# Kernel optimization log

Measured on AMD Instinct MI355X. Metric: run time of the kernel, lower is better.

## Reference

```python
import jax, jax.numpy as jnp
import numpy as np
import math

DIM = 4096
N_HEADS = 32
N_KV_HEADS = 8
HEAD_DIM = DIM // N_HEADS  # 128
ROPE_THETA = 500000.0
SEQ_LEN = 1
START_IDX = 8191
CACHE_LEN = START_IDX + SEQ_LEN  # 8192


def _rope(x, cos, sin):
    # x: [s, h, d]; cos/sin: [s, d//2]. Strided (even/odd) RoPE as in source.
    xe = x[:, :, 0::2]
    xo = x[:, :, 1::2]
    c = cos[:, None, :]
    s = sin[:, None, :]
    re = xe * c - xo * s
    ro = xe * s + xo * c
    # interleave back: [..., d//2, 2] -> [..., d]
    return jnp.stack([re, ro], axis=-1).reshape(x.shape)


def setup_inputs() -> dict:
    key = jax.random.key(0)
    ks = jax.random.split(key, 7)
    sc = 0.02
    return {
        "x": jax.random.normal(ks[0], (SEQ_LEN, DIM), jnp.float32),
        "wq": jax.random.normal(ks[1], (DIM, DIM), jnp.float32) * sc,
        "wk": jax.random.normal(ks[2], (N_KV_HEADS * HEAD_DIM, DIM), jnp.float32) * sc,
        "wv": jax.random.normal(ks[3], (N_KV_HEADS * HEAD_DIM, DIM), jnp.float32) * sc,
        "wo": jax.random.normal(ks[4], (DIM, DIM), jnp.float32) * sc,
        "k_cache": jax.random.normal(ks[5], (CACHE_LEN, N_KV_HEADS, HEAD_DIM), jnp.float32),
        "v_cache": jax.random.normal(ks[6], (CACHE_LEN, N_KV_HEADS, HEAD_DIM), jnp.float32),
        "start_idx": START_IDX,
    }


def reference(x, wq, wk, wv, wo, k_cache, v_cache, start_idx):
    seq_len = x.shape[0]
    # QKV projections (matmul with w.T as in source)
    Q = (x @ wq.T).reshape(seq_len, N_HEADS, HEAD_DIM)
    K = (x @ wk.T).reshape(seq_len, N_KV_HEADS, HEAD_DIM)
    V = (x @ wv.T).reshape(seq_len, N_KV_HEADS, HEAD_DIM)

    # RoPE frequencies for positions [start_idx, start_idx+seq_len)
    inv_freq = 1.0 / (ROPE_THETA ** (jnp.arange(0, HEAD_DIM, 2, dtype=jnp.float32) / HEAD_DIM))
    t = jnp.arange(start_idx, start_idx + seq_len, dtype=jnp.float32)
    freqs = t[:, None] * inv_freq[None, :]  # [s, d/2]
    cos, sin = jnp.cos(freqs), jnp.sin(freqs)

    Q = _rope(Q, cos, sin)
    K = _rope(K, cos, sin)

    # KV-cache append (start_idx is a static Python int)
    kc = jax.lax.dynamic_update_slice(k_cache, K, (start_idx, 0, 0))
    vc = jax.lax.dynamic_update_slice(v_cache, V, (start_idx, 0, 0))
    total = start_idx + seq_len
    keys = kc[:total]    # [T, kvh, d]
    values = vc[:total]

    rep = N_HEADS // N_KV_HEADS
    Kr = jnp.repeat(keys, rep, axis=1)    # [T, h, d] (repeat_interleave)
    Vr = jnp.repeat(values, rep, axis=1)

    scale = 1.0 / math.sqrt(HEAD_DIM)
    scores = jnp.einsum('qhd,khd->hqk', Q, Kr) * scale  # [h, s, T]

    if seq_len > 1:
        q_pos = jnp.arange(seq_len)[:, None] + start_idx
        k_pos = jnp.arange(total)[None, :]
        mask = jnp.where(k_pos > q_pos, jnp.float32(-jnp.inf), 0.0)
        scores = scores + mask[None, :, :]

    probs = jax.nn.softmax(scores.astype(jnp.float32), axis=-1).astype(Q.dtype)
    out = jnp.einsum('hqk,khd->qhd', probs, Vr).reshape(seq_len, N_HEADS * HEAD_DIM)
    return out @ wo.T
```

## Files before the change

kernel.cpp:

```cpp
#include <hip/hip_runtime.h>
#include <math.h>

#define DIM 4096
#define HD 128
#define NH 32
#define NKV 8
#define CACHE_LEN 8192
#define NCHUNK 64
#define CHUNK 128
#define SCALE 0.08838834764831845f

__global__ __launch_bounds__(256) void qkv_rope_kernel(
    const float* __restrict__ x, const float* __restrict__ wq,
    const float* __restrict__ wk, const float* __restrict__ wv,
    float* __restrict__ k_cache, float* __restrict__ v_cache,
    const int* __restrict__ start_idx_p, float* __restrict__ q_out)
{
    const int wave = threadIdx.x >> 6;
    const int lane = threadIdx.x & 63;
    const int row  = blockIdx.x * 4 + wave;

    const float* w;
    if (row < DIM)                w = wq + (size_t)row * DIM;
    else if (row < DIM + NKV*HD)  w = wk + (size_t)(row - DIM) * DIM;
    else                          w = wv + (size_t)(row - DIM - NKV*HD) * DIM;

    const float4* w4 = (const float4*)w;
    const float4* x4 = (const float4*)x;
    float acc = 0.f;
#pragma unroll
    for (int it = 0; it < DIM/4/64; ++it) {
        float4 a = w4[it*64 + lane];
        float4 b = x4[it*64 + lane];
        acc = fmaf(a.x, b.x, acc); acc = fmaf(a.y, b.y, acc);
        acc = fmaf(a.z, b.z, acc); acc = fmaf(a.w, b.w, acc);
    }
#pragma unroll
    for (int off = 32; off > 0; off >>= 1) acc += __shfl_down(acc, off);

    __shared__ float dots[4];
    if (lane == 0) dots[wave] = acc;
    __syncthreads();

    if (threadIdx.x < 2) {
        const int sidx = *start_idx_p;
        const int r0 = blockIdx.x * 4 + (int)threadIdx.x * 2;
        const float de = dots[threadIdx.x*2];
        const float dd = dots[threadIdx.x*2 + 1];
        if (r0 < DIM + NKV*HD) {
            const int local = (r0 < DIM) ? r0 : r0 - DIM;
            const int p = (local & (HD-1)) >> 1;
            const float te   = (float)pow(500000.0, (double)p * (1.0/64.0));
            const float invf = 1.0f / te;
            const float freq = (float)sidx * invf;
            const double ang = (double)freq;
            const float c = (float)cos(ang), s = (float)sin(ang);
            const float re = de * c - dd * s;
            const float ro = de * s + dd * c;
            if (r0 < DIM) {
                q_out[r0] = re; q_out[r0+1] = ro;
            } else {
                const size_t base = (size_t)sidx * (NKV*HD) + (size_t)(r0 - DIM);
                k_cache[base] = re; k_cache[base+1] = ro;
            }
        } else {
            const size_t base = (size_t)sidx * (NKV*HD) + (size_t)(r0 - DIM - NKV*HD);
            v_cache[base] = de; v_cache[base+1] = dd;
        }
    }
}

__global__ __launch_bounds__(256) void attn_partial_kernel(
    const float* __restrict__ q, const float* __restrict__ k_cache,
    const float* __restrict__ v_cache,
    float* __restrict__ part_acc,
    float* __restrict__ part_l)
{
    const int kv    = blockIdx.x >> 6;
    const int chunk = blockIdx.x & 63;
    const int wave  = threadIdx.x >> 6;
    const int lane  = threadIdx.x & 63;
    const int g  = lane >> 4;
    const int gl = lane & 15;

    float4 q0[4], q1[4];
#pragma unroll
    for (int hh = 0; hh < 4; ++hh) {
        const float* qb = q + (size_t)(kv*4 + hh) * HD;
        float4 a = *(const float4*)(qb + gl*4);
        float4 b = *(const float4*)(qb + 64 + gl*4);
        a.x *= SCALE; a.y *= SCALE; a.z *= SCALE; a.w *= SCALE;
        b.x *= SCALE; b.y *= SCALE; b.z *= SCALE; b.w *= SCALE;
        q0[hh] = a; q1[hh] = b;
    }

    float acc0[4][4] = {{0}}, acc1[4][4] = {{0}};
    float lsum[4] = {0.f, 0.f, 0.f, 0.f};

    const int pbase = chunk*CHUNK + wave*32 + g;
    for (int it = 0; it < 8; ++it) {
        const int pos = pbase + it*4;
        const float* kb = k_cache + ((size_t)pos*NKV + kv) * HD;
        float4 k0 = *(const float4*)(kb + gl*4);
        float4 k1 = *(const float4*)(kb + 64 + gl*4);
        float s[4];
#pragma unroll
        for (int hh = 0; hh < 4; ++hh) {
            float t;
            t = q0[hh].x*k0.x + q0[hh].y*k0.y + q0[hh].z*k0.z + q0[hh].w*k0.w;
            t += q1[hh].x*k1.x + q1[hh].y*k1.y + q1[hh].z*k1.z + q1[hh].w*k1.w;
            s[hh] = t;
        }
#pragma unroll
        for (int off = 1; off < 16; off <<= 1) {
#pragma unroll
            for (int hh = 0; hh < 4; ++hh) s[hh] += __shfl_xor(s[hh], off);
        }
        const float* vb = v_cache + ((size_t)pos*NKV + kv) * HD;
        float4 v0 = *(const float4*)(vb + gl*4);
        float4 v1 = *(const float4*)(vb + 64 + gl*4);
#pragma unroll
        for (int hh = 0; hh < 4; ++hh) {
            const float p = expf(s[hh]);
            lsum[hh] += p;
            acc0[hh][0] = fmaf(p, v0.x, acc0[hh][0]);
            acc0[hh][1] = fmaf(p, v0.y, acc0[hh][1]);
            acc0[hh][2] = fmaf(p, v0.z, acc0[hh][2]);
            acc0[hh][3] = fmaf(p, v0.w, acc0[hh][3]);
            acc1[hh][0] = fmaf(p, v1.x, acc1[hh][0]);
            acc1[hh][1] = fmaf(p, v1.y, acc1[hh][1]);
            acc1[hh][2] = fmaf(p, v1.z, acc1[hh][2]);
            acc1[hh][3] = fmaf(p, v1.w, acc1[hh][3]);
        }
    }

#pragma unroll
    for (int off = 16; off < 64; off <<= 1) {
#pragma unroll
        for (int hh = 0; hh < 4; ++hh) {
            lsum[hh] += __shfl_xor(lsum[hh], off);
#pragma unroll
            for (int j = 0; j < 4; ++j) {
                acc0[hh][j] += __shfl_xor(acc0[hh][j], off);
                acc1[hh][j] += __shfl_xor(acc1[hh][j], off);
            }
        }
    }

    __shared__ float red[4][4*HD];
    __shared__ float lred[4][4];
    if (lane < 16) {
#pragma unroll
        for (int hh = 0; hh < 4; ++hh) {
            *(float4*)&red[wave][hh*HD + gl*4] =
                make_float4(acc0[hh][0], acc0[hh][1], acc0[hh][2], acc0[hh][3]);
            *(float4*)&red[wave][hh*HD + 64 + gl*4] =
                make_float4(acc1[hh][0], acc1[hh][1], acc1[hh][2], acc1[hh][3]);
        }
        if (gl == 0) {
            lred[wave][0] = lsum[0]; lred[wave][1] = lsum[1];
            lred[wave][2] = lsum[2]; lred[wave][3] = lsum[3];
        }
    }
    __syncthreads();

    float* outp = part_acc + (size_t)blockIdx.x * (4*HD);
#pragma unroll
    for (int k = 0; k < 2; ++k) {
        const int idx = (int)threadIdx.x + k*256;
        outp[idx] = red[0][idx] + red[1][idx] + red[2][idx] + red[3][idx];
    }
    if (threadIdx.x < 4) {
        part_l[(size_t)blockIdx.x*4 + threadIdx.x] =
            lred[0][threadIdx.x] + lred[1][threadIdx.x] +
            lred[2][threadIdx.x] + lred[3][threadIdx.x];
    }
}

__global__ __launch_bounds__(128) void attn_combine_kernel(
    const float* __restrict__ part_acc, const float* __restrict__ part_l,
    float* __restrict__ attn_out)
{
    const int h  = blockIdx.x;
    const int kv = h >> 2, hh = h & 3;
    const int d  = threadIdx.x;
    float acc = 0.f, l = 0.f;
    for (int c = 0; c < NCHUNK; ++c) {
        const int pid = kv*NCHUNK + c;
        acc += part_acc[(size_t)pid*(4*HD) + hh*HD + d];
        l   += part_l[pid*4 + hh];
    }
    attn_out[h*HD + d] = acc / l;
}

__global__ __launch_bounds__(256) void out_proj_kernel(
    const float* __restrict__ attn, const float* __restrict__ wo,
    float* __restrict__ out)
{
    const int wave = threadIdx.x >> 6;
    const int lane = threadIdx.x & 63;
    const int row  = blockIdx.x * 4 + wave;
    const float4* w4 = (const float4*)(wo + (size_t)row * DIM);
    const float4* a4 = (const float4*)attn;
    float acc = 0.f;
#pragma unroll
    for (int it = 0; it < DIM/4/64; ++it) {
        float4 a = w4[it*64 + lane];
        float4 b = a4[it*64 + lane];
        acc = fmaf(a.x, b.x, acc); acc = fmaf(a.y, b.y, acc);
        acc = fmaf(a.z, b.z, acc); acc = fmaf(a.w, b.w, acc);
    }
#pragma unroll
    for (int off = 32; off > 0; off >>= 1) acc += __shfl_down(acc, off);
    if (lane == 0) out[row] = acc;
}

extern "C" void kernel_launch(void* const* d_in, const int* in_sizes, int n_in,
                              void* d_out, int out_size, void* d_ws, size_t ws_size,
                              hipStream_t stream)
{
    const float* x  = (const float*)d_in[0];
    const float* wq = (const float*)d_in[1];
    const float* wk = (const float*)d_in[2];
    const float* wv = (const float*)d_in[3];
    const float* wo = (const float*)d_in[4];
    float* k_cache  = (float*)d_in[5];
    float* v_cache  = (float*)d_in[6];
    const int* sidx = (const int*)d_in[7];
    float* out = (float*)d_out;

    float* ws       = (float*)d_ws;
    float* q        = ws;
    float* part_acc = ws + 4096;
    float* part_l   = part_acc + 512*512;
    float* attn     = part_l + 2048;

    hipLaunchKernelGGL(qkv_rope_kernel, dim3((DIM + NKV*HD*2)/4), dim3(256), 0, stream,
                       x, wq, wk, wv, k_cache, v_cache, sidx, q);
    hipLaunchKernelGGL(attn_partial_kernel, dim3(NKV*NCHUNK), dim3(256), 0, stream,
                       q, k_cache, v_cache, part_acc, part_l);
    hipLaunchKernelGGL(attn_combine_kernel, dim3(NH), dim3(HD), 0, stream,
                       part_acc, part_l, attn);
    hipLaunchKernelGGL(out_proj_kernel, dim3(DIM/4), dim3(256), 0, stream,
                       attn, wo, out);
}
```

Measured before the change: 238.5 us.

## Precompute RoPE table, split rows across waves, double attention chunks and prefetch KV

Adds a tiny kernel that computes the RoPE cos/sin table once, so QKV blocks no longer run double-precision pow/cos/sin per row pair. The QKV and output projections now split each row's dot product across more waves, using 2 or 1 rows per block to raise the number of blocks. The attention partial kernel doubles the number of chunks and halves their size, and loads K and V for two positions at once to expose more memory-level parallelism. The costs are an extra kernel launch, more partials for the combine step to read, and more shared-memory reductions.

```diff
diff --git a/kernel.cpp b/kernel.cpp
--- a/kernel.cpp
+++ b/kernel.cpp
@@ -6,30 +6,45 @@
 #define NH 32
 #define NKV 8
 #define CACHE_LEN 8192
-#define NCHUNK 64
-#define CHUNK 128
+#define NCHUNK 128
+#define CHUNK 64
 #define SCALE 0.08838834764831845f
+
+__global__ __launch_bounds__(64) void rope_table_kernel(
+    const int* __restrict__ start_idx_p, float* __restrict__ tab )
+{
+    const int p = threadIdx.x;
+    const float te   = (float)pow(500000.0, (double)p * (1.0/64.0));
+    const float invf = 1.0f / te;
+    const float freq = (float)(*start_idx_p) * invf;
+    const double ang = (double)freq;
+    tab[p]      = (float)cos(ang);
+    tab[64 + p] = (float)sin(ang);
+}
 
 __global__ __launch_bounds__(256) void qkv_rope_kernel(
     const float* __restrict__ x, const float* __restrict__ wq,
     const float* __restrict__ wk, const float* __restrict__ wv,
     float* __restrict__ k_cache, float* __restrict__ v_cache,
-    const int* __restrict__ start_idx_p, float* __restrict__ q_out)
+    const int* __restrict__ start_idx_p, const float* __restrict__ tab,
+    float* __restrict__ q_out)
 {
     const int wave = threadIdx.x >> 6;
     const int lane = threadIdx.x & 63;
-    const int row  = blockIdx.x * 4 + wave;
+    const int r0   = blockIdx.x * 2;
+    const int rrow = r0 + (wave >> 1);
+    const int sub  = wave & 1;
 
     const float* w;
-    if (row < DIM)                w = wq + (size_t)row * DIM;
-    else if (row < DIM + NKV*HD)  w = wk + (size_t)(row - DIM) * DIM;
-    else                          w = wv + (size_t)(row - DIM - NKV*HD) * DIM;
-
-    const float4* w4 = (const float4*)w;
-    const float4* x4 = (const float4*)x;
+    if (rrow < DIM)                w = wq + (size_t)rrow * DIM;
+    else if (rrow < DIM + NKV*HD)  w = wk + (size_t)(rrow - DIM) * DIM;
+    else                           w = wv + (size_t)(rrow - DIM - NKV*HD) * DIM;
+
+    const float4* w4 = (const float4*)w + sub*512;
+    const float4* x4 = (const float4*)x + sub*512;
     float acc = 0.f;
 #pragma unroll
-    for (int it = 0; it < DIM/4/64; ++it) {
+    for (int it = 0; it < 8; ++it) {
         float4 a = w4[it*64 + lane];
         float4 b = x4[it*64 + lane];
         acc = fmaf(a.x, b.x, acc); acc = fmaf(a.y, b.y, acc);
@@ -42,19 +57,14 @@
     if (lane == 0) dots[wave] = acc;
     __syncthreads();
 
-    if (threadIdx.x < 2) {
+    if (threadIdx.x == 0) {
+        const float de = dots[0] + dots[1];
+        const float dd = dots[2] + dots[3];
         const int sidx = *start_idx_p;
-        const int r0 = blockIdx.x * 4 + (int)threadIdx.x * 2;
-        const float de = dots[threadIdx.x*2];
-        const float dd = dots[threadIdx.x*2 + 1];
         if (r0 < DIM + NKV*HD) {
             const int local = (r0 < DIM) ? r0 : r0 - DIM;
             const int p = (local & (HD-1)) >> 1;
-            const float te   = (float)pow(500000.0, (double)p * (1.0/64.0));
-            const float invf = 1.0f / te;
-            const float freq = (float)sidx * invf;
-            const double ang = (double)freq;
-            const float c = (float)cos(ang), s = (float)sin(ang);
+            const float c = tab[p], s = tab[64 + p];
             const float re = de * c - dd * s;
             const float ro = de * s + dd * c;
             if (r0 < DIM) {
@@ -76,8 +86,8 @@
     float* __restrict__ part_acc,
     float* __restrict__ part_l)
 {
-    const int kv    = blockIdx.x >> 6;
-    const int chunk = blockIdx.x & 63;
+    const int kv    = blockIdx.x >> 7;
+    const int chunk = blockIdx.x & (NCHUNK-1);
     const int wave  = threadIdx.x >> 6;
     const int lane  = threadIdx.x & 63;
     const int g  = lane >> 4;
@@ -97,40 +107,55 @@
     float acc0[4][4] = {{0}}, acc1[4][4] = {{0}};
     float lsum[4] = {0.f, 0.f, 0.f, 0.f};
 
-    const int pbase = chunk*CHUNK + wave*32 + g;
-    for (int it = 0; it < 8; ++it) {
-        const int pos = pbase + it*4;
-        const float* kb = k_cache + ((size_t)pos*NKV + kv) * HD;
-        float4 k0 = *(const float4*)(kb + gl*4);
-        float4 k1 = *(const float4*)(kb + 64 + gl*4);
-        float s[4];
+    const int pbase = chunk*CHUNK + wave*16 + g*4;
+#pragma unroll
+    for (int it = 0; it < 4; it += 2) {
+        const int posA = pbase + it, posB = pbase + it + 1;
+        const float* kA = k_cache + ((size_t)posA*NKV + kv) * HD;
+        const float* kB = k_cache + ((size_t)posB*NKV + kv) * HD;
+        const float* vA = v_cache + ((size_t)posA*NKV + kv) * HD;
+        const float* vB = v_cache + ((size_t)posB*NKV + kv) * HD;
+        float4 k0A = *(const float4*)(kA + gl*4);
+        float4 k1A = *(const float4*)(kA + 64 + gl*4);
+        float4 k0B = *(const float4*)(kB + gl*4);
+        float4 k1B = *(const float4*)(kB + 64 + gl*4);
+        float4 v0A = *(const float4*)(vA + gl*4);
+        float4 v1A = *(const float4*)(vA + 64 + gl*4);
+        float4 v0B = *(const float4*)(vB + gl*4);
+        float4 v1B = *(const float4*)(vB + 64 + gl*4);
+
+        float sA[4], sB[4];
 #pragma unroll
         for (int hh = 0; hh < 4; ++hh) {
             float t;
-            t = q0[hh].x*k0.x + q0[hh].y*k0.y + q0[hh].z*k0.z + q0[hh].w*k0.w;
-            t += q1[hh].x*k1.x + q1[hh].y*k1.y + q1[hh].z*k1.z + q1[hh].w*k1.w;
-            s[hh] = t;
+            t  = q0[hh].x*k0A.x + q0[hh].y*k0A.y + q0[hh].z*k0A.z + q0[hh].w*k0A.w;
+            t += q1[hh].x*k1A.x + q1[hh].y*k1A.y + q1[hh].z*k1A.z + q1[hh].w*k1A.w;
+            sA[hh] = t;
+            t  = q0[hh].x*k0B.x + q0[hh].y*k0B.y + q0[hh].z*k0B.z + q0[hh].w*k0B.w;
+            t += q1[hh].x*k1B.x + q1[hh].y*k1B.y + q1[hh].z*k1B.z + q1[hh].w*k1B.w;
+            sB[hh] = t;
         }
 #pragma unroll
         for (int off = 1; off < 16; off <<= 1) {
 #pragma unroll
-            for (int hh = 0; hh < 4; ++hh) s[hh] += __shfl_xor(s[hh], off);
-        }
-        const float* vb = v_cache + ((size_t)pos*NKV + kv) * HD;
-        float4 v0 = *(const float4*)(vb + gl*4);
-        float4 v1 = *(const float4*)(vb + 64 + gl*4);
-#pragma unroll
-        for (int hh = 0; hh < 4; ++hh) {
-            const float p = expf(s[hh]);
-            lsum[hh] += p;
-            acc0[hh][0] = fmaf(p, v0.x, acc0[hh][0]);
-            acc0[hh][1] = fmaf(p, v0.y, acc0[hh][1]);
-            acc0[hh][2] = fmaf(p, v0.z, acc0[hh][2]);
-            acc0[hh][3] = fmaf(p, v0.w, acc0[hh][3]);
-            acc1[hh][0] = fmaf(p, v1.x, acc1[hh][0]);
-            acc1[hh][1] = fmaf(p, v1.y, acc1[hh][1]);
-            acc1[hh][2] = fmaf(p, v1.z, acc1[hh][2]);
-            acc1[hh][3] = fmaf(p, v1.w, acc1[hh][3]);
+            for (int hh = 0; hh < 4; ++hh) {
+                sA[hh] += __shfl_xor(sA[hh], off);
+                sB[hh] += __shfl_xor(sB[hh], off);
+            }
+        }
+#pragma unroll
+        for (int hh = 0; hh < 4; ++hh) {
+            const float pA = expf(sA[hh]);
+            const float pB = expf(sB[hh]);
+            lsum[hh] += pA + pB;
+            acc0[hh][0] = fmaf(pA, v0A.x, fmaf(pB, v0B.x, acc0[hh][0]));
+            acc0[hh][1] = fmaf(pA, v0A.y, fmaf(pB, v0B.y, acc0[hh][1]));
+            acc0[hh][2] = fmaf(pA, v0A.z, fmaf(pB, v0B.z, acc0[hh][2]));
+            acc0[hh][3] = fmaf(pA, v0A.w, fmaf(pB, v0B.w, acc0[hh][3]));
+            acc1[hh][0] = fmaf(pA, v1A.x, fmaf(pB, v1B.x, acc1[hh][0]));
+            acc1[hh][1] = fmaf(pA, v1A.y, fmaf(pB, v1B.y, acc1[hh][1]));
+            acc1[hh][2] = fmaf(pA, v1A.z, fmaf(pB, v1B.z, acc1[hh][2]));
+            acc1[hh][3] = fmaf(pA, v1A.w, fmaf(pB, v1B.w, acc1[hh][3]));
         }
     }
 
@@ -197,22 +222,23 @@
     const float* __restrict__ attn, const float* __restrict__ wo,
     float* __restrict__ out)
 {
-    const int wave = threadIdx.x >> 6;
-    const int lane = threadIdx.x & 63;
-    const int row  = blockIdx.x * 4 + wave;
+    const int row = blockIdx.x;
     const float4* w4 = (const float4*)(wo + (size_t)row * DIM);
     const float4* a4 = (const float4*)attn;
     float acc = 0.f;
 #pragma unroll
-    for (int it = 0; it < DIM/4/64; ++it) {
-        float4 a = w4[it*64 + lane];
-        float4 b = a4[it*64 + lane];
+    for (int it = 0; it < 4; ++it) {
+        float4 a = w4[it*256 + threadIdx.x];
+        float4 b = a4[it*256 + threadIdx.x];
         acc = fmaf(a.x, b.x, acc); acc = fmaf(a.y, b.y, acc);
         acc = fmaf(a.z, b.z, acc); acc = fmaf(a.w, b.w, acc);
     }
 #pragma unroll
     for (int off = 32; off > 0; off >>= 1) acc += __shfl_down(acc, off);
-    if (lane == 0) out[row] = acc;
+    __shared__ float dots[4];
+    if ((threadIdx.x & 63) == 0) dots[threadIdx.x >> 6] = acc;
+    __syncthreads();
+    if (threadIdx.x == 0) out[row] = dots[0] + dots[1] + dots[2] + dots[3];
 }
 
 extern "C" void kernel_launch(void* const* d_in, const int* in_sizes, int n_in,
@@ -232,15 +258,17 @@
     float* ws       = (float*)d_ws;
     float* q        = ws;
     float* part_acc = ws + 4096;
-    float* part_l   = part_acc + 512*512;
-    float* attn     = part_l + 2048;
-
-    hipLaunchKernelGGL(qkv_rope_kernel, dim3((DIM + NKV*HD*2)/4), dim3(256), 0, stream,
-                       x, wq, wk, wv, k_cache, v_cache, sidx, q);
+    float* part_l   = part_acc + 1024*512;
+    float* attn     = part_l + 4096;
+    float* tab      = attn + 4096;
+
+    hipLaunchKernelGGL(rope_table_kernel, dim3(1), dim3(64), 0, stream, sidx, tab);
+    hipLaunchKernelGGL(qkv_rope_kernel, dim3((DIM + NKV*HD*2)/2), dim3(256), 0, stream,
+                       x, wq, wk, wv, k_cache, v_cache, sidx, tab, q);
     hipLaunchKernelGGL(attn_partial_kernel, dim3(NKV*NCHUNK), dim3(256), 0, stream,
                        q, k_cache, v_cache, part_acc, part_l);
     hipLaunchKernelGGL(attn_combine_kernel, dim3(NH), dim3(HD), 0, stream,
                        part_acc, part_l, attn);
-    hipLaunchKernelGGL(out_proj_kernel, dim3(DIM/4), dim3(256), 0, stream,
+    hipLaunchKernelGGL(out_proj_kernel, dim3(DIM), dim3(256), 0, stream,
                        attn, wo, out);
 }
```

New measurement: 246.7 us. 1.03x slower.
